# Kernel tuning notes

Measured on AMD Instinct MI355X. Metric: run time of the kernel, lower is better.

Reference implementation:

```python
import jax, jax.numpy as jnp
import numpy as np

GROUP_SIZE = 128


def setup_inputs() -> dict:
    key = jax.random.key(0)
    k1, k2, k3, k4, k5, k6 = jax.random.split(key, 6)
    M, K, N = 8192, 4096, 11008
    num_groups = K // GROUP_SIZE  # 32
    x = (jax.random.normal(k1, (M, K), dtype=jnp.float32)).astype(jnp.float16)
    # packed uint8 bytes, each holding two int4 nibbles (stored as int32 for harness)
    packed_weight = jax.random.randint(k2, (N, K // 2), 0, 256, dtype=jnp.int32)
    # per-group, per-output-channel scales (positive, small) and zero points
    weight_scale = (jax.random.uniform(k3, (num_groups, N), dtype=jnp.float32) * 0.02 + 0.001).astype(jnp.float16)
    weight_zero = (jax.random.normal(k4, (num_groups, N), dtype=jnp.float32) * 0.5).astype(jnp.float16)
    # positive per-input-channel smoothing factors in a moderate range
    smooth_scale = (jax.random.uniform(k5, (K,), dtype=jnp.float32) * 1.5 + 0.5).astype(jnp.float16)
    bias = (jax.random.normal(k6, (N,), dtype=jnp.float32) * 0.02).astype(jnp.float16)
    return {"x": x, "packed_weight": packed_weight, "weight_scale": weight_scale,
            "weight_zero": weight_zero, "smooth_scale": smooth_scale, "bias": bias}


def _dequant_weight(packed_weight, weight_scale, weight_zero, K):
    # unpack two INT4 values per byte: even k -> low nibble, odd k -> high nibble
    low = (packed_weight & 15) - 8          # [N, K/2] int
    high = ((packed_weight >> 4) & 15) - 8  # [N, K/2] int
    N = packed_weight.shape[0]
    w_int = jnp.stack([low, high], axis=-1).reshape(N, -1)[:, :K]  # [N, K]
    # per-group dequant: group index along K
    g = jnp.arange(K) // GROUP_SIZE          # [K]
    scale = weight_scale[g]                  # [K, N] fp16
    zp = weight_zero[g]                      # [K, N] fp16
    # (q - zp) * scale, laid out [K, N] for x @ W
    return (w_int.astype(jnp.float16).T - zp) * scale


def reference(x, packed_weight, weight_scale, weight_zero, smooth_scale, bias):
    K = x.shape[-1]
    # per-channel smoothing of activations
    xs = (x / smooth_scale).astype(jnp.float16)           # [M, K]
    w_deq = _dequant_weight(packed_weight, weight_scale, weight_zero, K)  # [K, N]
    out = jnp.dot(xs, w_deq) + bias[None, :]              # [M, N] fp16
    return out.astype(jnp.float16)
```

## Files before the change

kernel.cpp:

```cpp
#include <hip/hip_runtime.h>
#include <hip/hip_fp16.h>

typedef _Float16 f16;
typedef _Float16 f16x8 __attribute__((ext_vector_type(8)));
typedef float f32x4 __attribute__((ext_vector_type(4)));
typedef int int4v __attribute__((ext_vector_type(4)));

#define BM 256
#define BN 256
#define NBUF 4
#define BUFSZ 32768

typedef const __attribute__((address_space(1))) unsigned int* gas_ptr;
typedef __attribute__((address_space(3))) unsigned int* las_ptr;

__device__ __forceinline__ void gload_lds16(const void* g, void* l) {
    __builtin_amdgcn_global_load_lds((gas_ptr)g, (las_ptr)l, 16, 0, 0);
}

__global__ __launch_bounds__(256) void quantx_kernel(
    const float* __restrict__ x, const float* __restrict__ smooth,
    char* __restrict__ Aq, float* __restrict__ sx, f16* __restrict__ U,
    int M, int K)
{
    const int row = blockIdx.x * 4 + (threadIdx.x >> 6);
    const int lane = threadIdx.x & 63;
    if (row >= M) return;

    f32x4 xsv[16];
    float amax = 0.f;
#pragma unroll
    for (int j = 0; j < 16; ++j) {
        const int k = j * 256 + lane * 4;
        const f32x4 xv = *(const f32x4*)(x + (size_t)row * K + k);
        const f32x4 sv = *(const f32x4*)(smooth + k);
        f32x4 r;
#pragma unroll
        for (int e = 0; e < 4; ++e) {
            r[e] = xv[e] / sv[e];
            amax = fmaxf(amax, fabsf(r[e]));
        }
        xsv[j] = r;
    }
#pragma unroll
    for (int off = 1; off < 64; off <<= 1)
        amax = fmaxf(amax, __shfl_xor(amax, off));
    const float sxr = fmaxf(amax, 1e-20f) / 127.f;
    const float inv = 127.f / fmaxf(amax, 1e-20f);
    if (lane == 0) sx[row] = sxr;

    int* aq32 = (int*)(Aq + (size_t)row * K);
#pragma unroll
    for (int j = 0; j < 16; ++j) {
        unsigned int pk = 0;
        float s4 = 0.f;
#pragma unroll
        for (int e = 0; e < 4; ++e) {
            const float v = xsv[j][e];
            s4 += v;
            int qi = (int)__builtin_rintf(v * inv);
            qi = qi > 127 ? 127 : (qi < -127 ? -127 : qi);
            pk |= ((unsigned int)(qi & 255)) << (8 * e);
        }
        aq32[j * 64 + lane] = (int)pk;
#pragma unroll
        for (int off = 1; off < 32; off <<= 1)
            s4 += __shfl_xor(s4, off);
        if ((lane & 31) == 0)
            U[(size_t)row * 32 + 2 * j + (lane >> 5)] = (f16)s4;
    }
}

__global__ __launch_bounds__(256) void repackw_kernel(
    const int* __restrict__ packed, char* __restrict__ Wq, int total8)
{
    const int i = blockIdx.x * 256 + threadIdx.x;
    if (i >= total8) return;
    const int4v p0 = *(const int4v*)(packed + i * 8);
    const int4v p1 = *(const int4v*)(packed + i * 8 + 4);
    int4v o;
#pragma unroll
    for (int w = 0; w < 4; ++w) {
        const int a = (w < 2) ? p0[2 * w] : p1[2 * (w - 2)];
        const int b = (w < 2) ? p0[2 * w + 1] : p1[2 * (w - 2) + 1];
        const int l0 = ((a & 15) - 8) & 255, h0 = (((a >> 4) & 15) - 8) & 255;
        const int l1 = ((b & 15) - 8) & 255, h1 = (((b >> 4) & 15) - 8) & 255;
        o[w] = l0 | (h0 << 8) | (l1 << 16) | (h1 << 24);
    }
    *(int4v*)(Wq + (size_t)i * 16) = o;
}

__global__ __launch_bounds__(256) void vneg_kernel(
    const float* __restrict__ wscale, const float* __restrict__ wzero,
    f16* __restrict__ Vneg, int N)
{
    const int i = blockIdx.x * 256 + threadIdx.x;
    if (i >= N * 32) return;
    const int n = i >> 5;
    const int g = i & 31;
    Vneg[i] = (f16)(-wscale[(size_t)g * N + n] * wzero[(size_t)g * N + n]);
}

__global__ __launch_bounds__(512, 2) void gemm_kernel(
    const char* __restrict__ Aq,
    const char* __restrict__ Wq,
    const float* __restrict__ wscale,
    const float* __restrict__ sx,
    const f16* __restrict__ U,
    const f16* __restrict__ Vneg,
    const float* __restrict__ bias,
    float* __restrict__ C,
    int M, int N, int K)
{
    __shared__ char lds[NBUF * BUFSZ];

    const int t = threadIdx.x;
    const int lane = t & 63;
    const int wid = t >> 6;
    const int wr = wid >> 2;
    const int wc = wid & 3;
    const int fr = lane & 15;
    const int fq = lane >> 4;

    const int nbm = M / BM;
    const int nbn = N / BN;
    const int nwg = nbm * nbn;
    const int bid = (int)blockIdx.x;

    int bm, bn;
    if (nbm == 32 && nbn == 43) {
        const int x = bid & 7, s = bid >> 3;
        const int r = s >> 5, q = s & 31;
        const int pos = (r < 5) ? (r * 256 + x * 32 + q)
                                : (1280 + x * 12 + (s - 160));
        int st, w;
        if (pos < 1024)      { st = pos >> 8; w = pos & 255; }
        else if (pos < 1200) { st = 4;        w = pos - 1024; }
        else                 { st = 5;        w = pos - 1200; }
        if (st < 4) { bm = (st & 1) * 16 + (w >> 4); bn = (st >> 1) * 16 + (w & 15); }
        else        { bm = (st & 1) * 16 + (w / 11); bn = 32 + (w % 11); }
    } else {
        const int cpx = nwg >> 3;
        const int wg = (bid & 7) * cpx + (bid >> 3);
        bm = wg % nbm; bn = wg / nbm;
    }
    const size_t m0 = (size_t)bm * BM;
    const size_t n0 = (size_t)bn * BN;

    const int scv = (t & 7) ^ ((t >> 3) & 7);
    const int rbase = 2 * (t >> 3) + (scv >> 2);
    const int kb = (scv & 3) * 16;
    const char* gAq = Aq + (m0 + rbase) * (size_t)K + kb;
    const char* gWq = Wq + (n0 + rbase) * (size_t)K + kb;

#define STAGE_A(sb, Tst) do { char* _d = lds + (sb) + t * 16; \
    gload_lds16(gAq + (size_t)(Tst) * 64, _d); \
    gload_lds16(gAq + (size_t)128 * K + (size_t)(Tst) * 64, _d + 8192); } while (0)
#define STAGE_B(sb, Tst) do { char* _d = lds + (sb) + 16384 + t * 16; \
    gload_lds16(gWq + (size_t)(Tst) * 64, _d); \
    gload_lds16(gWq + (size_t)128 * K + (size_t)(Tst) * 64, _d + 8192); } while (0)

    const int aswz = ((((fr & 1) << 2) | fq) ^ ((fr >> 1) & 7)) << 4;
    const int aBase = wr * 8192 + ((fr >> 1) << 7) + aswz;
    const int bBase = 16384 + wc * 4096 + ((fr >> 1) << 7) + aswz;

#define LDA(db, m) (*(const int4v*)(lds + (db) + aBase + (m) * 1024))
#define LDB(db, n) (*(const int4v*)(lds + (db) + bBase + (n) * 1024))

    f32x4 accf[8][4];
#pragma unroll
    for (int m = 0; m < 8; ++m)
#pragma unroll
        for (int n = 0; n < 4; ++n)
            accf[m][n] = {0.f, 0.f, 0.f, 0.f};

    const int4v kz = {0, 0, 0, 0};
    const int NG = K >> 7;

    STAGE_A(0, 0); STAGE_B(0, 0);
    STAGE_A(BUFSZ, 1); STAGE_B(BUFSZ, 1);
    float sgc[4];
#pragma unroll
    for (int n = 0; n < 4; ++n)
        sgc[n] = wscale[n0 + wc * 64 + n * 16 + fr];
    asm volatile("s_waitcnt vmcnt(0)" ::: "memory");
    __builtin_amdgcn_s_barrier();

#pragma unroll 1
    for (int g = 0; g < NG; ++g) {
        const int db0 = ((2 * g)     & 3) * BUFSZ;
        const int db1 = ((2 * g + 1) & 3) * BUFSZ;
        const bool hn = (g + 1) < NG;

        if (hn) {
            const int sb0 = ((2 * g + 2) & 3) * BUFSZ;
            const int sb1 = ((2 * g + 3) & 3) * BUFSZ;
            STAGE_A(sb0, 2 * g + 2); STAGE_B(sb0, 2 * g + 2);
            STAGE_A(sb1, 2 * g + 3); STAGE_B(sb1, 2 * g + 3);
        }
        float sgn[4] = {sgc[0], sgc[1], sgc[2], sgc[3]};
        if (hn) {
#pragma unroll
            for (int n = 0; n < 4; ++n)
                sgn[n] = wscale[(size_t)(g + 1) * N + n0 + wc * 64 + n * 16 + fr];
        }

        int4v a0[8], a1[8], b0[4], b1[4];
#pragma unroll
        for (int m = 0; m < 8; ++m) { a0[m] = LDA(db0, m); a1[m] = LDA(db1, m); }
#pragma unroll
        for (int n = 0; n < 4; ++n) { b0[n] = LDB(db0, n); b1[n] = LDB(db1, n); }

        __builtin_amdgcn_s_setprio(1);
#pragma unroll
        for (int m = 0; m < 8; ++m)
#pragma unroll
            for (int n = 0; n < 4; ++n) {
                int4v tv = __builtin_amdgcn_mfma_i32_16x16x64_i8(
                    a0[m], b0[n], kz, 0, 0, 0);
                tv = __builtin_amdgcn_mfma_i32_16x16x64_i8(
                    a1[m], b1[n], tv, 0, 0, 0);
#pragma unroll
                for (int e = 0; e < 4; ++e)
                    accf[m][n][e] += sgc[n] * (float)tv[e];
            }
        __builtin_amdgcn_s_setprio(0);

#pragma unroll
        for (int n = 0; n < 4; ++n) sgc[n] = sgn[n];

        asm volatile("s_waitcnt vmcnt(0)" ::: "memory");
        __builtin_amdgcn_s_barrier();
    }

#pragma unroll
    for (int m = 0; m < 8; ++m) {
        const f32x4 sxv = *(const f32x4*)(sx + m0 + wr * 128 + m * 16 + fq * 4);
#pragma unroll
        for (int n = 0; n < 4; ++n)
#pragma unroll
            for (int e = 0; e < 4; ++e)
                accf[m][n][e] *= sxv[e];
    }

    {
        f16x8 uf[8], vf[4];
#pragma unroll
        for (int m = 0; m < 8; ++m)
            uf[m] = *(const f16x8*)(U + (m0 + wr * 128 + m * 16 + fr) * 32 + fq * 8);
#pragma unroll
        for (int n = 0; n < 4; ++n)
            vf[n] = *(const f16x8*)(Vneg + (n0 + wc * 64 + n * 16 + fr) * 32 + fq * 8);
#pragma unroll
        for (int m = 0; m < 8; ++m)
#pragma unroll
            for (int n = 0; n < 4; ++n)
                accf[m][n] = __builtin_amdgcn_mfma_f32_16x16x32_f16(
                    uf[m], vf[n], accf[m][n], 0, 0, 0);
    }

#pragma unroll
    for (int n = 0; n < 4; ++n) {
        const size_t gcol = n0 + wc * 64 + n * 16 + fr;
        const float bv = bias[gcol];
#pragma unroll
        for (int am = 0; am < 8; ++am) {
            const size_t grow = m0 + wr * 128 + am * 16 + fq * 4;
#pragma unroll
            for (int r = 0; r < 4; ++r)
                C[(grow + r) * N + gcol] = accf[am][n][r] + bv;
        }
    }
}

extern "C" void kernel_launch(void* const* d_in, const int* in_sizes, int n_in,
                              void* d_out, int out_size, void* d_ws, size_t ws_size,
                              hipStream_t stream) {
    const float* x      = (const float*)d_in[0];
    const int* packed   = (const int*)d_in[1];
    const float* wscale = (const float*)d_in[2];
    const float* wzero  = (const float*)d_in[3];
    const float* smooth = (const float*)d_in[4];
    const float* bias   = (const float*)d_in[5];
    float* out = (float*)d_out;

    const int K = in_sizes[4];
    const int N = in_sizes[5];
    const int M = in_sizes[0] / K;
    const size_t MK = (size_t)M * K;
    const size_t NK = (size_t)N * K;

    char* Aq  = (char*)d_ws;
    char* Wq  = Aq + MK;
    f16* U    = (f16*)(Wq + NK);
    f16* Vneg = U + (size_t)M * 32;
    float* sxp = (float*)(Vneg + (size_t)N * 32);

    quantx_kernel<<<(M + 3) / 4, 256, 0, stream>>>(x, smooth, Aq, sxp, U, M, K);
    const int total8 = (int)(NK / 16);
    repackw_kernel<<<(total8 + 255) / 256, 256, 0, stream>>>(packed, Wq, total8);
    vneg_kernel<<<(N * 32 + 255) / 256, 256, 0, stream>>>(wscale, wzero, Vneg, N);

    const int grid_gemm = (M / BM) * (N / BN);
    gemm_kernel<<<grid_gemm, 512, 0, stream>>>(
        Aq, Wq, wscale, sxp, U, Vneg, bias, out, M, N, K);
}
```

Measured before the change: 694.7 us.

## Shrink GEMM tiles to 128x128 with triple-buffered single-step K pipeline

```diff
diff --git a/kernel.cpp b/kernel.cpp
--- a/kernel.cpp
+++ b/kernel.cpp
@@ -6,10 +6,10 @@
 typedef float f32x4 __attribute__((ext_vector_type(4)));
 typedef int int4v __attribute__((ext_vector_type(4)));
 
-#define BM 256
-#define BN 256
-#define NBUF 4
-#define BUFSZ 32768
+#define BM 128
+#define BN 128
+#define NBUF 3
+#define BUFSZ 16384
 
 typedef const __attribute__((address_space(1))) unsigned int* gas_ptr;
 typedef __attribute__((address_space(3))) unsigned int* las_ptr;
@@ -101,7 +101,7 @@
     Vneg[i] = (f16)(-wscale[(size_t)g * N + n] * wzero[(size_t)g * N + n]);
 }
 
-__global__ __launch_bounds__(512, 2) void gemm_kernel(
+__global__ __launch_bounds__(256, 3) void gemm_kernel(
     const char* __restrict__ Aq,
     const char* __restrict__ Wq,
     const float* __restrict__ wscale,
@@ -117,8 +117,8 @@
     const int t = threadIdx.x;
     const int lane = t & 63;
     const int wid = t >> 6;
-    const int wr = wid >> 2;
-    const int wc = wid & 3;
+    const int wr = wid >> 1;
+    const int wc = wid & 1;
     const int fr = lane & 15;
     const int fq = lane >> 4;
 
@@ -126,24 +126,10 @@
     const int nbn = N / BN;
     const int nwg = nbm * nbn;
     const int bid = (int)blockIdx.x;
-
-    int bm, bn;
-    if (nbm == 32 && nbn == 43) {
-        const int x = bid & 7, s = bid >> 3;
-        const int r = s >> 5, q = s & 31;
-        const int pos = (r < 5) ? (r * 256 + x * 32 + q)
-                                : (1280 + x * 12 + (s - 160));
-        int st, w;
-        if (pos < 1024)      { st = pos >> 8; w = pos & 255; }
-        else if (pos < 1200) { st = 4;        w = pos - 1024; }
-        else                 { st = 5;        w = pos - 1200; }
-        if (st < 4) { bm = (st & 1) * 16 + (w >> 4); bn = (st >> 1) * 16 + (w & 15); }
-        else        { bm = (st & 1) * 16 + (w / 11); bn = 32 + (w % 11); }
-    } else {
-        const int cpx = nwg >> 3;
-        const int wg = (bid & 7) * cpx + (bid >> 3);
-        bm = wg % nbm; bn = wg / nbm;
-    }
+    const int cpx = nwg >> 3;
+    const int wg = ((nwg & 7) == 0) ? ((bid & 7) * cpx + (bid >> 3)) : bid;
+    const int bm = wg % nbm;
+    const int bn = wg / nbm;
     const size_t m0 = (size_t)bm * BM;
     const size_t n0 = (size_t)bn * BN;
 
@@ -153,33 +139,32 @@
     const char* gAq = Aq + (m0 + rbase) * (size_t)K + kb;
     const char* gWq = Wq + (n0 + rbase) * (size_t)K + kb;
 
-#define STAGE_A(sb, Tst) do { char* _d = lds + (sb) + t * 16; \
+#define STAGE_AB(sb, Tst) do { char* _d = lds + (sb) + t * 16; \
     gload_lds16(gAq + (size_t)(Tst) * 64, _d); \
-    gload_lds16(gAq + (size_t)128 * K + (size_t)(Tst) * 64, _d + 8192); } while (0)
-#define STAGE_B(sb, Tst) do { char* _d = lds + (sb) + 16384 + t * 16; \
-    gload_lds16(gWq + (size_t)(Tst) * 64, _d); \
-    gload_lds16(gWq + (size_t)128 * K + (size_t)(Tst) * 64, _d + 8192); } while (0)
+    gload_lds16(gAq + (size_t)64 * K + (size_t)(Tst) * 64, _d + 4096); \
+    gload_lds16(gWq + (size_t)(Tst) * 64, _d + 8192); \
+    gload_lds16(gWq + (size_t)64 * K + (size_t)(Tst) * 64, _d + 12288); } while (0)
 
     const int aswz = ((((fr & 1) << 2) | fq) ^ ((fr >> 1) & 7)) << 4;
-    const int aBase = wr * 8192 + ((fr >> 1) << 7) + aswz;
-    const int bBase = 16384 + wc * 4096 + ((fr >> 1) << 7) + aswz;
+    const int aBase = wr * 4096 + ((fr >> 1) << 7) + aswz;
+    const int bBase = 8192 + wc * 4096 + ((fr >> 1) << 7) + aswz;
 
 #define LDA(db, m) (*(const int4v*)(lds + (db) + aBase + (m) * 1024))
 #define LDB(db, n) (*(const int4v*)(lds + (db) + bBase + (n) * 1024))
 
-    f32x4 accf[8][4];
-#pragma unroll
-    for (int m = 0; m < 8; ++m)
+    f32x4 accf[4][4];
+#pragma unroll
+    for (int m = 0; m < 4; ++m)
 #pragma unroll
         for (int n = 0; n < 4; ++n)
             accf[m][n] = {0.f, 0.f, 0.f, 0.f};
 
     const int4v kz = {0, 0, 0, 0};
-    const int NG = K >> 7;
-
-    STAGE_A(0, 0); STAGE_B(0, 0);
-    STAGE_A(BUFSZ, 1); STAGE_B(BUFSZ, 1);
-    float sgc[4];
+    const int NT = K >> 6;
+
+    STAGE_AB(0, 0);
+    STAGE_AB(BUFSZ, 1);
+    float sgc[4], sgn[4];
 #pragma unroll
     for (int n = 0; n < 4; ++n)
         sgc[n] = wscale[n0 + wc * 64 + n * 16 + fr];
@@ -187,55 +172,48 @@
     __builtin_amdgcn_s_barrier();
 
 #pragma unroll 1
-    for (int g = 0; g < NG; ++g) {
-        const int db0 = ((2 * g)     & 3) * BUFSZ;
-        const int db1 = ((2 * g + 1) & 3) * BUFSZ;
-        const bool hn = (g + 1) < NG;
-
-        if (hn) {
-            const int sb0 = ((2 * g + 2) & 3) * BUFSZ;
-            const int sb1 = ((2 * g + 3) & 3) * BUFSZ;
-            STAGE_A(sb0, 2 * g + 2); STAGE_B(sb0, 2 * g + 2);
-            STAGE_A(sb1, 2 * g + 3); STAGE_B(sb1, 2 * g + 3);
-        }
-        float sgn[4] = {sgc[0], sgc[1], sgc[2], sgc[3]};
-        if (hn) {
+    for (int T = 0; T < NT; ++T) {
+        const int db = (T % 3) * BUFSZ;
+        const int sb = ((T + 2) % 3) * BUFSZ;
+
+        if (T + 2 < NT) STAGE_AB(sb, T + 2);
+        if ((T & 1) && (T >> 1) + 1 < 32) {
 #pragma unroll
             for (int n = 0; n < 4; ++n)
-                sgn[n] = wscale[(size_t)(g + 1) * N + n0 + wc * 64 + n * 16 + fr];
-        }
-
-        int4v a0[8], a1[8], b0[4], b1[4];
-#pragma unroll
-        for (int m = 0; m < 8; ++m) { a0[m] = LDA(db0, m); a1[m] = LDA(db1, m); }
-#pragma unroll
-        for (int n = 0; n < 4; ++n) { b0[n] = LDB(db0, n); b1[n] = LDB(db1, n); }
+                sgn[n] = wscale[(size_t)((T >> 1) + 1) * N + n0 + wc * 64 + n * 16 + fr];
+        }
+
+        int4v bfr[4];
+#pragma unroll
+        for (int n = 0; n < 4; ++n) bfr[n] = LDB(db, n);
 
         __builtin_amdgcn_s_setprio(1);
 #pragma unroll
-        for (int m = 0; m < 8; ++m)
+        for (int m = 0; m < 4; ++m) {
+            const int4v av = LDA(db, m);
 #pragma unroll
             for (int n = 0; n < 4; ++n) {
-                int4v tv = __builtin_amdgcn_mfma_i32_16x16x64_i8(
-                    a0[m], b0[n], kz, 0, 0, 0);
-                tv = __builtin_amdgcn_mfma_i32_16x16x64_i8(
-                    a1[m], b1[n], tv, 0, 0, 0);
+                const int4v tv = __builtin_amdgcn_mfma_i32_16x16x64_i8(
+                    av, bfr[n], kz, 0, 0, 0);
 #pragma unroll
                 for (int e = 0; e < 4; ++e)
                     accf[m][n][e] += sgc[n] * (float)tv[e];
             }
+        }
         __builtin_amdgcn_s_setprio(0);
 
-#pragma unroll
-        for (int n = 0; n < 4; ++n) sgc[n] = sgn[n];
+        if (T & 1) {
+#pragma unroll
+            for (int n = 0; n < 4; ++n) sgc[n] = sgn[n];
+        }
 
         asm volatile("s_waitcnt vmcnt(0)" ::: "memory");
         __builtin_amdgcn_s_barrier();
     }
 
 #pragma unroll
-    for (int m = 0; m < 8; ++m) {
-        const f32x4 sxv = *(const f32x4*)(sx + m0 + wr * 128 + m * 16 + fq * 4);
+    for (int m = 0; m < 4; ++m) {
+        const f32x4 sxv = *(const f32x4*)(sx + m0 + wr * 64 + m * 16 + fq * 4);
 #pragma unroll
         for (int n = 0; n < 4; ++n)
 #pragma unroll
@@ -244,15 +222,15 @@
     }
 
     {
-        f16x8 uf[8], vf[4];
-#pragma unroll
-        for (int m = 0; m < 8; ++m)
-            uf[m] = *(const f16x8*)(U + (m0 + wr * 128 + m * 16 + fr) * 32 + fq * 8);
+        f16x8 uf[4], vf[4];
+#pragma unroll
+        for (int m = 0; m < 4; ++m)
+            uf[m] = *(const f16x8*)(U + (m0 + wr * 64 + m * 16 + fr) * 32 + fq * 8);
 #pragma unroll
         for (int n = 0; n < 4; ++n)
             vf[n] = *(const f16x8*)(Vneg + (n0 + wc * 64 + n * 16 + fr) * 32 + fq * 8);
 #pragma unroll
-        for (int m = 0; m < 8; ++m)
+        for (int m = 0; m < 4; ++m)
 #pragma unroll
             for (int n = 0; n < 4; ++n)
                 accf[m][n] = __builtin_amdgcn_mfma_f32_16x16x32_f16(
@@ -264,8 +242,8 @@
         const size_t gcol = n0 + wc * 64 + n * 16 + fr;
         const float bv = bias[gcol];
 #pragma unroll
-        for (int am = 0; am < 8; ++am) {
-            const size_t grow = m0 + wr * 128 + am * 16 + fq * 4;
+        for (int am = 0; am < 4; ++am) {
+            const size_t grow = m0 + wr * 64 + am * 16 + fq * 4;
 #pragma unroll
             for (int r = 0; r < 4; ++r)
                 C[(grow + r) * N + gcol] = accf[am][n][r] + bv;
@@ -302,6 +280,6 @@
     vneg_kernel<<<(N * 32 + 255) / 256, 256, 0, stream>>>(wscale, wzero, Vneg, N);
 
     const int grid_gemm = (M / BM) * (N / BN);
-    gemm_kernel<<<grid_gemm, 512, 0, stream>>>(
+    gemm_kernel<<<grid_gemm, 256, 0, stream>>>(
         Aq, Wq, wscale, sxp, U, Vneg, bias, out, M, N, K);
 }
```

Result: slower. 745.8 us (+7.4%).

## Load GEMM operands directly from global memory instead of staging through LDS

Applied to the files above, without the earlier changes.

```diff
diff --git a/kernel.cpp b/kernel.cpp
--- a/kernel.cpp
+++ b/kernel.cpp
@@ -8,15 +8,6 @@
 
 #define BM 256
 #define BN 256
-#define NBUF 4
-#define BUFSZ 32768
-
-typedef const __attribute__((address_space(1))) unsigned int* gas_ptr;
-typedef __attribute__((address_space(3))) unsigned int* las_ptr;
-
-__device__ __forceinline__ void gload_lds16(const void* g, void* l) {
-    __builtin_amdgcn_global_load_lds((gas_ptr)g, (las_ptr)l, 16, 0, 0);
-}
 
 __global__ __launch_bounds__(256) void quantx_kernel(
     const float* __restrict__ x, const float* __restrict__ smooth,
@@ -112,8 +103,6 @@
     float* __restrict__ C,
     int M, int N, int K)
 {
-    __shared__ char lds[NBUF * BUFSZ];
-
     const int t = threadIdx.x;
     const int lane = t & 63;
     const int wid = t >> 6;
@@ -147,25 +136,8 @@
     const size_t m0 = (size_t)bm * BM;
     const size_t n0 = (size_t)bn * BN;
 
-    const int scv = (t & 7) ^ ((t >> 3) & 7);
-    const int rbase = 2 * (t >> 3) + (scv >> 2);
-    const int kb = (scv & 3) * 16;
-    const char* gAq = Aq + (m0 + rbase) * (size_t)K + kb;
-    const char* gWq = Wq + (n0 + rbase) * (size_t)K + kb;
-
-#define STAGE_A(sb, Tst) do { char* _d = lds + (sb) + t * 16; \
-    gload_lds16(gAq + (size_t)(Tst) * 64, _d); \
-    gload_lds16(gAq + (size_t)128 * K + (size_t)(Tst) * 64, _d + 8192); } while (0)
-#define STAGE_B(sb, Tst) do { char* _d = lds + (sb) + 16384 + t * 16; \
-    gload_lds16(gWq + (size_t)(Tst) * 64, _d); \
-    gload_lds16(gWq + (size_t)128 * K + (size_t)(Tst) * 64, _d + 8192); } while (0)
-
-    const int aswz = ((((fr & 1) << 2) | fq) ^ ((fr >> 1) & 7)) << 4;
-    const int aBase = wr * 8192 + ((fr >> 1) << 7) + aswz;
-    const int bBase = 16384 + wc * 4096 + ((fr >> 1) << 7) + aswz;
-
-#define LDA(db, m) (*(const int4v*)(lds + (db) + aBase + (m) * 1024))
-#define LDB(db, n) (*(const int4v*)(lds + (db) + bBase + (n) * 1024))
+    const char* pA = Aq + (m0 + wr * 128 + fr) * (size_t)K + fq * 16;
+    const char* pW = Wq + (n0 + wc * 64 + fr) * (size_t)K + fq * 16;
 
     f32x4 accf[8][4];
 #pragma unroll
@@ -177,39 +149,25 @@
     const int4v kz = {0, 0, 0, 0};
     const int NG = K >> 7;
 
-    STAGE_A(0, 0); STAGE_B(0, 0);
-    STAGE_A(BUFSZ, 1); STAGE_B(BUFSZ, 1);
-    float sgc[4];
-#pragma unroll
-    for (int n = 0; n < 4; ++n)
-        sgc[n] = wscale[n0 + wc * 64 + n * 16 + fr];
-    asm volatile("s_waitcnt vmcnt(0)" ::: "memory");
-    __builtin_amdgcn_s_barrier();
-
 #pragma unroll 1
     for (int g = 0; g < NG; ++g) {
-        const int db0 = ((2 * g)     & 3) * BUFSZ;
-        const int db1 = ((2 * g + 1) & 3) * BUFSZ;
-        const bool hn = (g + 1) < NG;
-
-        if (hn) {
-            const int sb0 = ((2 * g + 2) & 3) * BUFSZ;
-            const int sb1 = ((2 * g + 3) & 3) * BUFSZ;
-            STAGE_A(sb0, 2 * g + 2); STAGE_B(sb0, 2 * g + 2);
-            STAGE_A(sb1, 2 * g + 3); STAGE_B(sb1, 2 * g + 3);
-        }
-        float sgn[4] = {sgc[0], sgc[1], sgc[2], sgc[3]};
-        if (hn) {
-#pragma unroll
-            for (int n = 0; n < 4; ++n)
-                sgn[n] = wscale[(size_t)(g + 1) * N + n0 + wc * 64 + n * 16 + fr];
-        }
+        const size_t kb0 = (size_t)g * 128;
 
         int4v a0[8], a1[8], b0[4], b1[4];
 #pragma unroll
-        for (int m = 0; m < 8; ++m) { a0[m] = LDA(db0, m); a1[m] = LDA(db1, m); }
-#pragma unroll
-        for (int n = 0; n < 4; ++n) { b0[n] = LDB(db0, n); b1[n] = LDB(db1, n); }
+        for (int m = 0; m < 8; ++m) {
+            a0[m] = *(const int4v*)(pA + (size_t)m * 16 * K + kb0);
+            a1[m] = *(const int4v*)(pA + (size_t)m * 16 * K + kb0 + 64);
+        }
+#pragma unroll
+        for (int n = 0; n < 4; ++n) {
+            b0[n] = *(const int4v*)(pW + (size_t)n * 16 * K + kb0);
+            b1[n] = *(const int4v*)(pW + (size_t)n * 16 * K + kb0 + 64);
+        }
+        float sgc[4];
+#pragma unroll
+        for (int n = 0; n < 4; ++n)
+            sgc[n] = wscale[(size_t)g * N + n0 + wc * 64 + n * 16 + fr];
 
         __builtin_amdgcn_s_setprio(1);
 #pragma unroll
@@ -225,12 +183,6 @@
                     accf[m][n][e] += sgc[n] * (float)tv[e];
             }
         __builtin_amdgcn_s_setprio(0);
-
-#pragma unroll
-        for (int n = 0; n < 4; ++n) sgc[n] = sgn[n];
-
-        asm volatile("s_waitcnt vmcnt(0)" ::: "memory");
-        __builtin_amdgcn_s_barrier();
     }
 
 #pragma unroll
```

After: 1.188 ms. 71.0% more time.
